# Performance work log

Hardware: AMD Instinct MI355X
Metric: run time of the kernel (lower is better)

## Reference

```python
import jax, jax.numpy as jnp
import numpy as np

B, T, D = 4, 1024, 2048      # batch, tokens, d_model (= Linear out_features)
N, S, H = 8, 8, 8            # n_concepts, gate_rank, degen_rank
ETA = 1.0


def setup_inputs() -> dict:
    key = jax.random.key(0)
    ks = jax.random.split(key, 9)
    return {
        "x": jax.random.normal(ks[0], (B, T, D), jnp.float32),
        # selector params (kaiming-ish then / d_model^2 -> small); use /D for nontrivial values
        "select_weight": jax.random.normal(ks[1], (N, D, S), jnp.float32) / D,
        "select_mean_diff": jax.random.normal(ks[2], (N, D), jnp.float32) / D,
        "imp_center": jax.random.normal(ks[3], (N,), jnp.float32),
        "imp_slope": jax.random.normal(ks[4], (N,), jnp.float32) * 5.0,
        "lora_update": jax.random.normal(ks[5], (N, D, H), jnp.float32) * 0.02,
        "lora_degen": jax.random.normal(ks[6], (N, D, H), jnp.float32) * 0.02,
        "bias_w": jax.random.normal(ks[7], (N, D), jnp.float32) * 0.02,
        "debias_w": jax.random.normal(ks[8], (N, D), jnp.float32) * 0.02,
    }


def reference(x, select_weight, select_mean_diff, imp_center, imp_slope,
              lora_update, lora_degen, bias_w, debias_w):
    # ---- SimpleSelectorOutProp ----
    # x: [B,T,D]; x_diff: [B,N,T,D]  (x.unsqueeze(1) - mean_diff[None,:,None,:])
    x_diff = x[:, None, :, :] - select_mean_diff[None, :, None, :]
    x_diff = x_diff / jnp.linalg.norm(x_diff, axis=3, keepdims=True)
    # cont: [B,N,T,S] = einsum('nds,bntd->bnts')**2
    cont = jnp.einsum('nds,bntd->bnts', select_weight, x_diff) ** 2
    score = cont.sum(axis=-1)                                   # [B,N,T]
    gate = jax.nn.sigmoid(imp_slope[None, :, None] * (score - imp_center[None, :, None]))
    sel_scale = gate.max(axis=1)[..., None]                     # [B,T,1] (max over concepts)
    sel_idx = gate.argmax(axis=1)                               # [B,T] int (top-1 concept)

    # ---- top-1 concept gather + low-rank update ----
    debias = jnp.take(debias_w, sel_idx, axis=0)                # [B,T,D]
    bias = jnp.take(bias_w, sel_idx, axis=0)                    # [B,T,D]
    upd = jnp.take(lora_update, sel_idx, axis=0)                # [B,T,D,H]
    dgn = jnp.take(lora_degen, sel_idx, axis=0)                 # [B,T,D,H]

    x_debias = x - debias
    mod_x = jnp.einsum('btdh,btd->bth', upd, x_debias)          # [B,T,H]
    degen_up = jnp.einsum('btdh,bth->btd', dgn, mod_x)          # [B,T,D]
    mod_x_bias = ETA * (bias + degen_up)

    # gated residual blend: (1 - s) * x + s * mod_x_bias
    return (1.0 - sel_scale) * x + sel_scale * mod_x_bias
```

## Files before the change

### kernel.cpp

```cpp
#include <hip/hip_runtime.h>
#include <math.h>

typedef unsigned short u16;
typedef unsigned int   u32;
typedef unsigned long long u64;
typedef __attribute__((ext_vector_type(4))) unsigned short u16x4;
typedef __attribute__((ext_vector_type(8))) unsigned short bf16x8;
typedef __attribute__((ext_vector_type(8))) short sh8;
typedef __attribute__((ext_vector_type(4))) float f32x4;

#define BT     4096
#define D      2048
#define NC     8
#define NCOL   144
#define NW     8
#define KR     (D / NW)
#define TPB    16
#define LPAD   (NCOL + 4)

__device__ __forceinline__ float bf2f(u16 v) {
    u32 u = ((u32)v) << 16;
    float f; __builtin_memcpy(&f, &u, 4); return f;
}
__device__ __forceinline__ u16 f2bf(float f) {
    u32 u; __builtin_memcpy(&u, &f, 4);
    u += 0x7fffu + ((u >> 16) & 1);
    return (u16)(u >> 16);
}

__device__ __forceinline__ int detect_fp32(const void* xv) {
    const u16* p = (const u16*)xv;
    int l = threadIdx.x & 63;
    bool bad = false;
#pragma unroll
    for (int i = 0; i < 4; i++) {
        float v = bf2f(p[l * 4 + i]);
        if (!(fabsf(v) < 1e4f)) bad = true;
    }
    return __ballot(bad) != 0ull;
}

template<int DT> struct IO;
template<> struct IO<0> {
    static __device__ __forceinline__ float ld1(const void* p, size_t i) {
        return bf2f(((const u16*)p)[i]);
    }
    static __device__ __forceinline__ void ld4(const void* p, size_t i, float* o) {
        u16x4 v = *(const u16x4*)((const u16*)p + i);
#pragma unroll
        for (int k = 0; k < 4; k++) o[k] = bf2f(v[k]);
    }
    static __device__ __forceinline__ void ld8(const void* p, size_t i, float* o) {
        bf16x8 v = *(const bf16x8*)((const u16*)p + i);
#pragma unroll
        for (int k = 0; k < 8; k++) o[k] = bf2f(v[k]);
    }
    static __device__ __forceinline__ void st4(void* p, size_t i, const float* v) {
        u16x4 o;
#pragma unroll
        for (int k = 0; k < 4; k++) o[k] = f2bf(v[k]);
        *(u16x4*)((u16*)p + i) = o;
    }
    static __device__ __forceinline__ u16 ldbf(const void* p, size_t i) {
        return ((const u16*)p)[i];
    }
    static __device__ __forceinline__ sh8 afrag(const void* p, size_t i) {
        return *(const sh8*)((const u16*)p + i);
    }
};
template<> struct IO<1> {
    static __device__ __forceinline__ float ld1(const void* p, size_t i) {
        return ((const float*)p)[i];
    }
    static __device__ __forceinline__ void ld4(const void* p, size_t i, float* o) {
        f32x4 a = *(const f32x4*)((const float*)p + i);
#pragma unroll
        for (int k = 0; k < 4; k++) o[k] = a[k];
    }
    static __device__ __forceinline__ void ld8(const void* p, size_t i, float* o) {
        f32x4 a = *(const f32x4*)((const float*)p + i);
        f32x4 b = *(const f32x4*)((const float*)p + i + 4);
#pragma unroll
        for (int k = 0; k < 4; k++) { o[k] = a[k]; o[4 + k] = b[k]; }
    }
    static __device__ __forceinline__ void st4(void* p, size_t i, const float* v) {
        f32x4 a;
#pragma unroll
        for (int k = 0; k < 4; k++) a[k] = v[k];
        *(f32x4*)((float*)p + i) = a;
    }
    static __device__ __forceinline__ u16 ldbf(const void* p, size_t i) {
        return f2bf(((const float*)p)[i]);
    }
    static __device__ __forceinline__ sh8 afrag(const void* p, size_t i) {
        f32x4 a = *(const f32x4*)((const float*)p + i);
        f32x4 b = *(const f32x4*)((const float*)p + i + 4);
        sh8 r;
#pragma unroll
        for (int k = 0; k < 4; k++) {
            r[k]     = (short)f2bf(a[k]);
            r[4 + k] = (short)f2bf(b[k]);
        }
        return r;
    }
};

template<int DT>
__device__ __forceinline__ void prep_part(const void* selW, const void* upd,
                                          const void* mu, u16* __restrict__ WtT) {
    int idx = blockIdx.x * 256 + threadIdx.x;
    int j = idx >> 8, d0 = (idx & 255) * 8;
    bf16x8 v;
    if (j < 64) {
        int n = j >> 3, s = j & 7;
#pragma unroll
        for (int i = 0; i < 8; i++) v[i] = IO<DT>::ldbf(selW, ((size_t)n * D + d0 + i) * 8 + s);
    } else if (j < 128) {
        int n = (j - 64) >> 3, h = j & 7;
#pragma unroll
        for (int i = 0; i < 8; i++) v[i] = IO<DT>::ldbf(upd, ((size_t)n * D + d0 + i) * 8 + h);
    } else if (j < 136) {
#pragma unroll
        for (int i = 0; i < 8; i++) v[i] = IO<DT>::ldbf(mu, (size_t)(j - 128) * D + d0 + i);
    } else {
#pragma unroll
        for (int i = 0; i < 8; i++) v[i] = 0;
    }
    int ct = j >> 4, m = j & 15;
    int w  = d0 >> 8, ks = (d0 >> 5) & 7, q = (d0 >> 3) & 3;
    size_t dst = ((((size_t)(w * 8 + ks) * 9 + ct) * 64) + q * 16 + m) * 8;
    *(bf16x8*)(WtT + dst) = v;
}

template<int DT>
__device__ __forceinline__ void consts_part(const void* W, const void* mu,
                                            const void* upd, const void* deb,
                                            float* __restrict__ gPart) {
    int pid = blockIdx.x - 144;
    int n = pid >> 3, t = threadIdx.x;
    int d = (pid & 7) * 256 + t;

    float mud = IO<DT>::ld1(mu,  (size_t)n * D + d);
    float dbd = IO<DT>::ld1(deb, (size_t)n * D + d);
    float m2 = mud * mud;
    float wv[8], uv[8], o[8], u[8];
    IO<DT>::ld8(W,   ((size_t)n * D + d) * 8, wv);
    IO<DT>::ld8(upd, ((size_t)n * D + d) * 8, uv);
#pragma unroll
    for (int s = 0; s < 8; s++) { o[s] = wv[s] * mud; u[s] = uv[s] * dbd; }

#pragma unroll
    for (int i = 1; i < 64; i <<= 1) {
        m2 += __shfl_xor(m2, i, 64);
#pragma unroll
        for (int s = 0; s < 8; s++) {
            o[s] += __shfl_xor(o[s], i, 64);
            u[s] += __shfl_xor(u[s], i, 64);
        }
    }
    __shared__ float red[4][17];
    int wave = t >> 6, lane = t & 63;
    if (lane == 0) {
        red[wave][0] = m2;
#pragma unroll
        for (int s = 0; s < 8; s++) { red[wave][1 + s] = o[s]; red[wave][9 + s] = u[s]; }
    }
    __syncthreads();
    if (t < 17) {
        float acc = red[0][t] + red[1][t] + red[2][t] + red[3][t];
        gPart[pid * 17 + t] = acc;
    }
}

template<int DT>
__device__ __forceinline__ void dgnb_part(const void* dgn, u16* __restrict__ dgnb) {
    int idx = (blockIdx.x - 208) * 256 + threadIdx.x;
    float v[8];
    IO<DT>::ld8(dgn, (size_t)idx * 8, v);
    bf16x8 o;
#pragma unroll
    for (int k = 0; k < 8; k++) o[k] = f2bf(v[k]);
    *(bf16x8*)(dgnb + (size_t)idx * 8) = o;
}

__global__ __launch_bounds__(256) void k_prep(
    const void* x, const void* selW, const void* upd, const void* mu,
    const void* deb, const void* dgn, u16* WtT, float* gPart, u16* dgnb) {
    int f = detect_fp32(x);
    if (blockIdx.x < 144) {
        if (f) prep_part<1>(selW, upd, mu, WtT); else prep_part<0>(selW, upd, mu, WtT);
    } else if (blockIdx.x < 208) {
        if (f) consts_part<1>(selW, mu, upd, deb, gPart);
        else   consts_part<0>(selW, mu, upd, deb, gPart);
    } else {
        if (f) dgnb_part<1>(dgn, dgnb); else dgnb_part<0>(dgn, dgnb);
    }
}

template<int DT>
__device__ __forceinline__ void fused_body(
    const void* X, const u16* __restrict__ WtT, const float* __restrict__ gPart,
    const u16* __restrict__ DGNB, const void* BIAS,
    const void* CENTER, const void* SLOPE, void* OUT,
    float (*LP)[TPB][LPAD], float (*LS2)[TPB],
    float (*cOFF)[8], float (*cUB)[8], float* cMU2,
    float (*mxL)[8], float* svalL, int* cL) {

    const int t = threadIdx.x;
    const int w = t >> 6, l = t & 63;
    const int m = l & 15, q = l >> 4;
    const int tok0 = blockIdx.x * TPB;
    const int k0 = w * KR;

    if (t < 136) {
        int n = t / 17, k = t % 17;
        float s = 0.f;
#pragma unroll
        for (int j = 0; j < 8; j++) s += gPart[(n * 8 + j) * 17 + k];
        if (k == 0)      cMU2[n] = s;
        else if (k < 9)  cOFF[n][k - 1] = s;
        else             cUB[n][k - 9] = s;
    }

    const size_t aoff = (size_t)(tok0 + m) * D + k0 + q * 8;
    const u16* bp = WtT + (size_t)w * (8 * 9 * 512) + (size_t)l * 8;

    f32x4 acc[9];
#pragma unroll
    for (int ct = 0; ct < 9; ct++) acc[ct] = (f32x4){0.f, 0.f, 0.f, 0.f};
    float s2 = 0.f;

#pragma unroll 2
    for (int ks = 0; ks < KR / 32; ks++) {
        sh8 a = IO<DT>::afrag(X, aoff + ks * 32);
        sh8 b[9];
#pragma unroll
        for (int ct = 0; ct < 9; ct++)
            b[ct] = *(const sh8*)(bp + (size_t)(ks * 9 + ct) * 512);
#pragma unroll
        for (int i = 0; i < 8; i++) {
            float xv = bf2f((u16)a[i]);
            s2 = fmaf(xv, xv, s2);
        }
#pragma unroll
        for (int ct = 0; ct < 9; ct++)
            acc[ct] = __builtin_amdgcn_mfma_f32_16x16x32_bf16(a, b[ct], acc[ct], 0, 0, 0);
    }

    s2 += __shfl_xor(s2, 16, 64);
    s2 += __shfl_xor(s2, 32, 64);
    if (l < 16) LS2[w][l] = s2;

#pragma unroll
    for (int ct = 0; ct < 9; ct++)
#pragma unroll
        for (int r = 0; r < 4; r++)
            LP[w][q * 4 + r][ct * 16 + m] = acc[ct][r];
    __syncthreads();

    if (t < 128) {
        const int tok = t >> 3, n = t & 7;
        float sx2 = 0.f;
#pragma unroll
        for (int u = 0; u < NW; u++) sx2 += LS2[u][tok];

        float pa[8];
#pragma unroll
        for (int s = 0; s < 8; s++) {
            float v = 0.f;
#pragma unroll
            for (int u = 0; u < NW; u++) v += LP[u][tok][n * 8 + s];
            pa[s] = v;
        }
        float mdot = 0.f;
#pragma unroll
        for (int u = 0; u < NW; u++) mdot += LP[u][tok][128 + n];

        float norm2 = sx2 - 2.f * mdot + cMU2[n];
        float sc = 0.f;
#pragma unroll
        for (int s = 0; s < 8; s++) {
            float dd = pa[s] - cOFF[n][s];
            sc += dd * dd;
        }
        sc /= norm2;
        float zv = IO<DT>::ld1(SLOPE, n) * (sc - IO<DT>::ld1(CENTER, n));
        int iv = n;
#pragma unroll
        for (int i = 1; i < 8; i <<= 1) {
            float z2 = __shfl_xor(zv, i, 64);
            int   i2 = __shfl_xor(iv, i, 64);
            if (z2 > zv || (z2 == zv && i2 < iv)) { zv = z2; iv = i2; }
        }
        const int c = iv;
        float mxv = 0.f;
#pragma unroll
        for (int u = 0; u < NW; u++) mxv += LP[u][tok][64 + c * 8 + n];
        mxL[tok][n] = mxv - cUB[c][n];
        if (n == 0) { svalL[tok] = 1.f / (1.f + expf(-zv)); cL[tok] = c; }
    }
    __syncthreads();

    const int d0 = t * 4;
    for (int tok = 0; tok < TPB; ++tok) {
        const int c = cL[tok];
        const float sval = svalL[tok];
        float mxa[8];
#pragma unroll
        for (int h = 0; h < 8; h++) mxa[h] = mxL[tok][h];

        const size_t trow = (size_t)(tok0 + tok) * D;
        float xf[4], bv[4], ov[4];
        IO<DT>::ld4(X,    trow + d0, xf);
        IO<DT>::ld4(BIAS, (size_t)c * D + d0, bv);
#pragma unroll
        for (int i = 0; i < 4; i++) {
            bf16x8 v = *(const bf16x8*)(DGNB + ((size_t)c * D + d0 + i) * 8);
            float du = bf2f(v[0]) * mxa[0] + bf2f(v[1]) * mxa[1]
                     + bf2f(v[2]) * mxa[2] + bf2f(v[3]) * mxa[3]
                     + bf2f(v[4]) * mxa[4] + bf2f(v[5]) * mxa[5]
                     + bf2f(v[6]) * mxa[6] + bf2f(v[7]) * mxa[7];
            ov[i] = (1.f - sval) * xf[i] + sval * (bv[i] + du);
        }
        IO<DT>::st4(OUT, trow + d0, ov);
    }
}

__global__ __launch_bounds__(512, 2) void k_fused(
    const void* X, const u16* WtT, const float* gPart, const u16* DGNB,
    const void* BIAS, const void* CENTER, const void* SLOPE, void* OUT) {
    __shared__ float LP[NW][TPB][LPAD];
    __shared__ float LS2[NW][TPB];
    __shared__ float cOFF[8][8], cUB[8][8], cMU2[8];
    __shared__ float mxL[TPB][8], svalL[TPB];
    __shared__ int   cL[TPB];
    if (detect_fp32(X))
        fused_body<1>(X, WtT, gPart, DGNB, BIAS, CENTER, SLOPE, OUT,
                      LP, LS2, cOFF, cUB, cMU2, mxL, svalL, cL);
    else
        fused_body<0>(X, WtT, gPart, DGNB, BIAS, CENTER, SLOPE, OUT,
                      LP, LS2, cOFF, cUB, cMU2, mxL, svalL, cL);
}

extern "C" void kernel_launch(void* const* d_in, const int* in_sizes, int n_in,
                              void* d_out, int out_size, void* d_ws, size_t ws_size,
                              hipStream_t stream) {
    const void* x      = d_in[0];
    const void* selW   = d_in[1];
    const void* mu     = d_in[2];
    const void* center = d_in[3];
    const void* slope  = d_in[4];
    const void* upd    = d_in[5];
    const void* dgn    = d_in[6];
    const void* biasW  = d_in[7];
    const void* debW   = d_in[8];

    char* ws = (char*)d_ws;
    u16*   WtT   = (u16*)ws;
    u16*   dgnb  = (u16*)(ws + 589824);
    float* gPart = (float*)(ws + 851968);

    k_prep <<<272, 256, 0, stream>>>(x, selW, upd, mu, debW, dgn, WtT, gPart, dgnb);
    k_fused<<<BT / TPB, 512, 0, stream>>>(x, WtT, gPart, dgnb, biasW, center, slope, d_out);
}
```

Measured before the change: 118.9 us.

## Double-buffer B fragments via global_load_lds with manual vmcnt pipelining

The MFMA B operand tiles are now streamed from global memory straight into a per-wave double-buffered LDS slab using global_load_lds, and the next step's X fragment is prefetched into registers, with explicit s_waitcnt vmcnt so loads overlap compute. The LDS slab is reused afterwards for the partial-sum exchange, and the constants reduction is moved after the main loop. The goal is to hide global load latency in the K loop. The hand-counted vmcnt values are fragile, and there is no barrier between the LDS reads of the last buffer and the reuse of the slab as LP. That reuse is per wave, though, so it may be safe.

```diff
diff --git a/kernel.cpp b/kernel.cpp
--- a/kernel.cpp
+++ b/kernel.cpp
@@ -18,6 +18,10 @@
 #define TPB    16
 #define LPAD   (NCOL + 4)
 
+#define FRAGU  512
+#define BUFU   (9 * FRAGU)
+#define SLABU  (2 * BUFU)
+
 __device__ __forceinline__ float bf2f(u16 v) {
     u32 u = ((u32)v) << 16;
     float f; __builtin_memcpy(&f, &u, 4); return f;
@@ -64,9 +68,6 @@
     static __device__ __forceinline__ u16 ldbf(const void* p, size_t i) {
         return ((const u16*)p)[i];
     }
-    static __device__ __forceinline__ sh8 afrag(const void* p, size_t i) {
-        return *(const sh8*)((const u16*)p + i);
-    }
 };
 template<> struct IO<1> {
     static __device__ __forceinline__ float ld1(const void* p, size_t i) {
@@ -91,17 +92,6 @@
     }
     static __device__ __forceinline__ u16 ldbf(const void* p, size_t i) {
         return f2bf(((const float*)p)[i]);
-    }
-    static __device__ __forceinline__ sh8 afrag(const void* p, size_t i) {
-        f32x4 a = *(const f32x4*)((const float*)p + i);
-        f32x4 b = *(const f32x4*)((const float*)p + i + 4);
-        sh8 r;
-#pragma unroll
-        for (int k = 0; k < 4; k++) {
-            r[k]     = (short)f2bf(a[k]);
-            r[4 + k] = (short)f2bf(b[k]);
-        }
-        return r;
     }
 };
 
@@ -197,12 +187,17 @@
     }
 }
 
+#define GLL16(gp, lp)                                                          \
+    __builtin_amdgcn_global_load_lds(                                          \
+        (const __attribute__((address_space(1))) u32*)(gp),                    \
+        (__attribute__((address_space(3))) u32*)(lp), 16, 0, 0)
+
 template<int DT>
 __device__ __forceinline__ void fused_body(
     const void* X, const u16* __restrict__ WtT, const float* __restrict__ gPart,
     const u16* __restrict__ DGNB, const void* BIAS,
     const void* CENTER, const void* SLOPE, void* OUT,
-    float (*LP)[TPB][LPAD], float (*LS2)[TPB],
+    u16* BS, float (*LS2)[TPB],
     float (*cOFF)[8], float (*cUB)[8], float* cMU2,
     float (*mxL)[8], float* svalL, int* cL) {
 
@@ -212,50 +207,93 @@
     const int tok0 = blockIdx.x * TPB;
     const int k0 = w * KR;
 
-    if (t < 136) {
-        int n = t / 17, k = t % 17;
-        float s = 0.f;
-#pragma unroll
-        for (int j = 0; j < 8; j++) s += gPart[(n * 8 + j) * 17 + k];
-        if (k == 0)      cMU2[n] = s;
-        else if (k < 9)  cOFF[n][k - 1] = s;
-        else             cUB[n][k - 9] = s;
-    }
-
     const size_t aoff = (size_t)(tok0 + m) * D + k0 + q * 8;
-    const u16* bp = WtT + (size_t)w * (8 * 9 * 512) + (size_t)l * 8;
+    const u16* gB = WtT + (size_t)w * (8 * 9 * FRAGU);
+    u16* sB = BS + w * SLABU;
 
     f32x4 acc[9];
 #pragma unroll
     for (int ct = 0; ct < 9; ct++) acc[ct] = (f32x4){0.f, 0.f, 0.f, 0.f};
     float s2 = 0.f;
 
-#pragma unroll 2
-    for (int ks = 0; ks < KR / 32; ks++) {
-        sh8 a = IO<DT>::afrag(X, aoff + ks * 32);
-        sh8 b[9];
-#pragma unroll
-        for (int ct = 0; ct < 9; ct++)
-            b[ct] = *(const sh8*)(bp + (size_t)(ks * 9 + ct) * 512);
+    f32x4 r0C = {}, r1C = {}, r0N = {}, r1N = {};
+    sh8 aCr = {}, aNr = {};
+
+#pragma unroll
+    for (int ct = 0; ct < 9; ct++)
+        GLL16(gB + ct * FRAGU + l * 8, sB + ct * FRAGU);
+    if constexpr (DT) {
+        r0C = *(const f32x4*)((const float*)X + aoff);
+        r1C = *(const f32x4*)((const float*)X + aoff + 4);
+    } else {
+        aCr = *(const sh8*)((const u16*)X + aoff);
+    }
+
+#pragma unroll
+    for (int k = 0; k < KR / 32; k++) {
+        if (k < KR / 32 - 1) {
+            const u16* g1 = gB + (size_t)(k + 1) * (9 * FRAGU);
+            u16* s1 = sB + ((k + 1) & 1) * BUFU;
+#pragma unroll
+            for (int ct = 0; ct < 9; ct++)
+                GLL16(g1 + ct * FRAGU + l * 8, s1 + ct * FRAGU);
+            if constexpr (DT) {
+                r0N = *(const f32x4*)((const float*)X + aoff + (k + 1) * 32);
+                r1N = *(const f32x4*)((const float*)X + aoff + (k + 1) * 32 + 4);
+            } else {
+                aNr = *(const sh8*)((const u16*)X + aoff + (k + 1) * 32);
+            }
+            if constexpr (DT) asm volatile("s_waitcnt vmcnt(11)" ::: "memory");
+            else              asm volatile("s_waitcnt vmcnt(10)" ::: "memory");
+        } else {
+            asm volatile("s_waitcnt vmcnt(0)" ::: "memory");
+        }
+
+        sh8 a;
+        if constexpr (DT) {
+#pragma unroll
+            for (int i = 0; i < 4; i++) {
+                a[i]     = (short)f2bf(r0C[i]);
+                a[4 + i] = (short)f2bf(r1C[i]);
+            }
+        } else {
+            a = aCr;
+        }
 #pragma unroll
         for (int i = 0; i < 8; i++) {
             float xv = bf2f((u16)a[i]);
             s2 = fmaf(xv, xv, s2);
         }
-#pragma unroll
-        for (int ct = 0; ct < 9; ct++)
-            acc[ct] = __builtin_amdgcn_mfma_f32_16x16x32_bf16(a, b[ct], acc[ct], 0, 0, 0);
+        const u16* bb = sB + (k & 1) * BUFU;
+#pragma unroll
+        for (int ct = 0; ct < 9; ct++) {
+            sh8 b = *(const sh8*)(bb + ct * FRAGU + l * 8);
+            acc[ct] = __builtin_amdgcn_mfma_f32_16x16x32_bf16(a, b, acc[ct], 0, 0, 0);
+        }
+        if constexpr (DT) { r0C = r0N; r1C = r1N; }
+        else              { aCr = aNr; }
     }
 
     s2 += __shfl_xor(s2, 16, 64);
     s2 += __shfl_xor(s2, 32, 64);
     if (l < 16) LS2[w][l] = s2;
 
+    float* LPw = (float*)(BS + w * SLABU);
 #pragma unroll
     for (int ct = 0; ct < 9; ct++)
 #pragma unroll
         for (int r = 0; r < 4; r++)
-            LP[w][q * 4 + r][ct * 16 + m] = acc[ct][r];
+            LPw[(q * 4 + r) * LPAD + ct * 16 + m] = acc[ct][r];
+
+    if (t < 136) {
+        int n = t / 17, kk = t % 17;
+        float s = 0.f;
+#pragma unroll
+        for (int j = 0; j < 8; j++) s += gPart[(n * 8 + j) * 17 + kk];
+        if (kk == 0)      cMU2[n] = s;
+        else if (kk < 9)  cOFF[n][kk - 1] = s;
+        else              cUB[n][kk - 9] = s;
+    }
     __syncthreads();
 
     if (t < 128) {
@@ -269,12 +307,14 @@
         for (int s = 0; s < 8; s++) {
             float v = 0.f;
 #pragma unroll
-            for (int u = 0; u < NW; u++) v += LP[u][tok][n * 8 + s];
+            for (int u = 0; u < NW; u++)
+                v += ((const float*)(BS + u * SLABU))[tok * LPAD + n * 8 + s];
             pa[s] = v;
         }
         float mdot = 0.f;
 #pragma unroll
-        for (int u = 0; u < NW; u++) mdot += LP[u][tok][128 + n];
+        for (int u = 0; u < NW; u++)
+            mdot += ((const float*)(BS + u * SLABU))[tok * LPAD + 128 + n];
 
         float norm2 = sx2 - 2.f * mdot + cMU2[n];
         float sc = 0.f;
@@ -295,7 +335,8 @@
         const int c = iv;
         float mxv = 0.f;
 #pragma unroll
-        for (int u = 0; u < NW; u++) mxv += LP[u][tok][64 + c * 8 + n];
+        for (int u = 0; u < NW; u++)
+            mxv += ((const float*)(BS + u * SLABU))[tok * LPAD + 64 + c * 8 + n];
         mxL[tok][n] = mxv - cUB[c][n];
         if (n == 0) { svalL[tok] = 1.f / (1.f + expf(-zv)); cL[tok] = c; }
     }
@@ -329,17 +370,17 @@
 __global__ __launch_bounds__(512, 2) void k_fused(
     const void* X, const u16* WtT, const float* gPart, const u16* DGNB,
     const void* BIAS, const void* CENTER, const void* SLOPE, void* OUT) {
-    __shared__ float LP[NW][TPB][LPAD];
+    __shared__ __align__(16) u16 BS[NW * SLABU];
     __shared__ float LS2[NW][TPB];
     __shared__ float cOFF[8][8], cUB[8][8], cMU2[8];
     __shared__ float mxL[TPB][8], svalL[TPB];
     __shared__ int   cL[TPB];
     if (detect_fp32(X))
         fused_body<1>(X, WtT, gPart, DGNB, BIAS, CENTER, SLOPE, OUT,
-                      LP, LS2, cOFF, cUB, cMU2, mxL, svalL, cL);
+                      BS, LS2, cOFF, cUB, cMU2, mxL, svalL, cL);
     else
         fused_body<0>(X, WtT, gPart, DGNB, BIAS, CENTER, SLOPE, OUT,
-                      LP, LS2, cOFF, cUB, cMU2, mxL, svalL, cL);
+                      BS, LS2, cOFF, cUB, cMU2, mxL, svalL, cL);
 }
 
 extern "C" void kernel_launch(void* const* d_in, const int* in_sizes, int n_in,
```

Result: faster. 115.8 us (-2.6%).
